# Performance work log

Measured on AMD Instinct MI355X. Metric: run time of the kernel, lower is better.

## Reference

```python
import jax, jax.numpy as jnp
import numpy as np

NEG = 0.01  # leaky_relu negative slope used throughout AttentiveFP


def _seg_softmax(logits, seg, num):
    # softmax over entries grouped by segment id (PyG softmax w/ 1e-16 eps)
    m = jax.ops.segment_max(logits, seg, num_segments=num)
    m = jnp.where(jnp.isfinite(m), m, 0.0)
    e = jnp.exp(logits - m[seg])
    s = jax.ops.segment_sum(e, seg, num_segments=num)
    return e / (s[seg] + 1e-16)


def _gru(x, h, wi, wh, bi, bh):
    # torch.nn.GRUCell math
    gi = x @ wi.T + bi
    gh = h @ wh.T + bh
    ir, iz, inn = jnp.split(gi, 3, axis=-1)
    hr, hz, hn = jnp.split(gh, 3, axis=-1)
    r = jax.nn.sigmoid(ir + hr)
    z = jax.nn.sigmoid(iz + hz)
    n = jnp.tanh(inn + r * hn)
    return (1.0 - z) * n + z * h


def _forward(x, edge_attr, mol_feats, lin1_w, lin1_b, gate_lin1_w, gate_lin2_w, gate_att_l, gate_att_r, gate_bias, grus_wi, grus_wh, grus_bi, grus_bh, atom_w, atom_att_src, atom_att_dst, atom_bias, mol_w, mol_att_src, mol_att_dst, mol_bias, lin2_w, lin2_b, fcm0_w, fcm0_b, fcm1_w, fcm1_b, fcm2_w, fcm2_b, fc0_w, fc0_b, fc1_w, fc1_b, fc2_w, fc2_b, fc3_w, fc3_b, fc4_w, fc4_b, edge_index, batch):
    N = x.shape[0]
    G = mol_feats.shape[0]
    src, dst = edge_index[0], edge_index[1]
    lrelu = lambda v: jax.nn.leaky_relu(v, NEG)
    # AttentiveFP (eval mode: dropout off)
    xh = lrelu(x @ lin1_w.T + lin1_b)  # [N,H]
    # --- GATEConv: edge-conditioned attention, add aggregation ---
    m = lrelu(jnp.concatenate([xh[src], edge_attr], axis=-1) @ gate_lin1_w.T)  # [E,H]
    a = lrelu(m @ gate_att_l + (xh @ gate_att_r)[dst])
    a = _seg_softmax(a, dst, N)
    h = jax.ops.segment_sum((m @ gate_lin2_w.T) * a[:, None], dst, num_segments=N) + gate_bias
    xh = jax.nn.relu(_gru(jax.nn.elu(h), xh, grus_wi[0], grus_wh[0], grus_bi[0], grus_bh[0]))
    # --- GATConv layers (num_layers-1 = 2, heads=1, no self loops) ---
    for l in range(2):
        xl = xh @ atom_w[l].T
        a = lrelu((xl @ atom_att_src[l])[src] + (xl @ atom_att_dst[l])[dst])
        a = _seg_softmax(a, dst, N)
        h = jax.ops.segment_sum(xl[src] * a[:, None], dst, num_segments=N) + atom_bias[l]
        xh = jax.nn.relu(_gru(jax.nn.elu(h), xh, grus_wi[1 + l], grus_wh[1 + l], grus_bi[1 + l], grus_bh[1 + l]))
    # --- attentive graph readout (num_timesteps = 3) ---
    out = jax.nn.relu(jax.ops.segment_sum(xh, batch, num_segments=G))  # [G,H]
    xm = xh @ mol_w.T            # atom-side lin (x fixed across timesteps)
    a_src = xm @ mol_att_src
    for _ in range(3):
        a = lrelu(a_src + ((out @ mol_w.T) @ mol_att_dst)[batch])
        a = _seg_softmax(a, batch, G)
        h = jax.ops.segment_sum(xm * a[:, None], batch, num_segments=G) + mol_bias
        out = jax.nn.relu(_gru(jax.nn.elu(h), out, grus_wi[3], grus_wh[3], grus_bi[3], grus_bh[3]))
    hg = out @ lin2_w.T + lin2_b  # [G,256]
    # --- mol-feature MLP branch (SiLU) ---
    hm = jax.nn.silu(mol_feats @ fcm0_w.T + fcm0_b)
    hm = jax.nn.silu(hm @ fcm1_w.T + fcm1_b)
    hm = jax.nn.silu(hm @ fcm2_w.T + fcm2_b)
    # --- fusion MLP ---
    hg = jnp.concatenate([hg, hm], axis=1)  # [G,512]
    hg = jax.nn.silu(hg @ fc0_w.T + fc0_b)
    hg = jax.nn.silu(hg @ fc1_w.T + fc1_b)
    hg = jax.nn.silu(hg @ fc2_w.T + fc2_b)
    hg = jax.nn.silu(hg @ fc3_w.T + fc3_b)
    return hg @ fc4_w.T + fc4_b  # [G,1]


def setup_inputs() -> dict:
    key = jax.random.key(0)
    ks = iter(jax.random.split(key, 64))
    def W(*shape):
        return jax.random.normal(next(ks), shape, jnp.float32) / np.float32(np.sqrt(shape[-1]))
    def B(*shape):
        return 0.02 * jax.random.normal(next(ks), shape, jnp.float32)
    N, E, G = 131072, 262144, 8192
    Fn, Fe, Fm, H = 64, 16, 200, 256
    return dict(
        x=jax.random.normal(next(ks), (N, Fn), jnp.float32),
        edge_attr=jax.random.normal(next(ks), (E, Fe), jnp.float32),
        mol_feats=jax.random.normal(next(ks), (G, Fm), jnp.float32),
        lin1_w=W(H, Fn), lin1_b=B(H),
        gate_lin1_w=W(H, H + Fe), gate_lin2_w=W(H, H),
        gate_att_l=W(H), gate_att_r=W(H), gate_bias=B(H),
        grus_wi=W(4, 3 * H, H), grus_wh=W(4, 3 * H, H), grus_bi=B(4, 3 * H), grus_bh=B(4, 3 * H),
        atom_w=W(2, H, H), atom_att_src=W(2, H), atom_att_dst=W(2, H), atom_bias=B(2, H),
        mol_w=W(H, H), mol_att_src=W(H), mol_att_dst=W(H), mol_bias=B(H),
        lin2_w=W(H, H), lin2_b=B(H),
        fcm0_w=W(H, Fm), fcm0_b=B(H), fcm1_w=W(H, H), fcm1_b=B(H), fcm2_w=W(H, H), fcm2_b=B(H),
        fc0_w=W(512, 512), fc0_b=B(512), fc1_w=W(512, 512), fc1_b=B(512),
        fc2_w=W(512, 512), fc2_b=B(512), fc3_w=W(128, 512), fc3_b=B(128),
        fc4_w=W(1, 128), fc4_b=B(1),
        edge_index=jax.random.randint(next(ks), (2, E), 0, N),
        batch=jnp.sort(jax.random.randint(next(ks), (N,), 0, G)),
    )


def reference(x, edge_attr, mol_feats, lin1_w, lin1_b, gate_lin1_w, gate_lin2_w, gate_att_l, gate_att_r, gate_bias, grus_wi, grus_wh, grus_bi, grus_bh, atom_w, atom_att_src, atom_att_dst, atom_bias, mol_w, mol_att_src, mol_att_dst, mol_bias, lin2_w, lin2_b, fcm0_w, fcm0_b, fcm1_w, fcm1_b, fcm2_w, fcm2_b, fc0_w, fc0_b, fc1_w, fc1_b, fc2_w, fc2_b, fc3_w, fc3_b, fc4_w, fc4_b, edge_index, batch):
    return _forward(x, edge_attr, mol_feats, lin1_w, lin1_b, gate_lin1_w, gate_lin2_w, gate_att_l, gate_att_r, gate_bias, grus_wi, grus_wh, grus_bi, grus_bh, atom_w, atom_att_src, atom_att_dst, atom_bias, mol_w, mol_att_src, mol_att_dst, mol_bias, lin2_w, lin2_b, fcm0_w, fcm0_b, fcm1_w, fcm1_b, fcm2_w, fcm2_b, fc0_w, fc0_b, fc1_w, fc1_b, fc2_w, fc2_b, fc3_w, fc3_b, fc4_w, fc4_b, edge_index, batch)
```

## Files before the change

kernel.cpp:

```cpp
#include <hip/hip_runtime.h>
#include <hip/hip_bf16.h>
#include <math.h>


typedef unsigned short u16;
typedef u16 u16x8 __attribute__((ext_vector_type(8)));
typedef short s16x8 __attribute__((ext_vector_type(8)));
typedef float f32x4 __attribute__((ext_vector_type(4)));

__device__ __forceinline__ float u2f(u16 u) { return __uint_as_float(((unsigned)u) << 16); }
__device__ __forceinline__ u16 f2u(float f) {
    return __builtin_bit_cast(u16, __float2bfloat16(f));
}

#define NEGS 0.01f

__device__ __forceinline__ unsigned fkey(float f) {
    unsigned u = __float_as_uint(f);
    return (u & 0x80000000u) ? ~u : (u | 0x80000000u);
}
__device__ __forceinline__ float funkey(unsigned k) {
    return (k & 0x80000000u) ? __uint_as_float(k ^ 0x80000000u) : __uint_as_float(~k);
}
#define KEY_NEG_INF 0x007FFFFFu

static inline int cdiv(int a, int b) { return (a + b - 1) / b; }

__global__ void fill_f32(float* p, float v, size_t n) {
    size_t i = (size_t)blockIdx.x * 256 + threadIdx.x;
    if (i < n) p[i] = v;
}
__global__ void fill_u32(unsigned* p, unsigned v, int n) {
    int i = blockIdx.x * 256 + threadIdx.x;
    if (i < n) p[i] = v;
}
__global__ void copy_f2b(const float* s, u16* d, size_t n) {
    size_t i = (size_t)blockIdx.x * 256 + threadIdx.x;
    if (i < n) d[i] = f2u(s[i]);
}
__global__ void copy_u32(const unsigned* s, unsigned* d, int n) {
    int i = blockIdx.x * 256 + threadIdx.x;
    if (i < n) d[i] = s[i];
}
__global__ void matvecT_k(const float* W, const float* a, float* v, int K, int Jout) {
    int j = blockIdx.x * 256 + threadIdx.x;
    if (j >= Jout) return;
    float s = 0.f;
    for (int k = 0; k < K; k++) s += W[(size_t)k * Jout + j] * a[k];
    v[j] = s;
}
__global__ void edge_add_lrelu(float* elog, const float* r, const int* dsti, int E) {
    int i = blockIdx.x * 256 + threadIdx.x;
    if (i < E) {
        float v = elog[i] + r[dsti[i]];
        elog[i] = v > 0.f ? v : NEGS * v;
    }
}
__global__ void pair_logit(float* elog, const float* s, const float* d,
                           const int* srci, const int* dsti, int E) {
    int i = blockIdx.x * 256 + threadIdx.x;
    if (i < E) {
        float v = s[srci[i]] + d[dsti[i]];
        elog[i] = v > 0.f ? v : NEGS * v;
    }
}
__global__ void node_logit(float* nlog, const float* asrc, const float* wg,
                           const int* batch, int N) {
    int i = blockIdx.x * 256 + threadIdx.x;
    if (i < N) {
        float v = asrc[i] + wg[batch[i]];
        nlog[i] = v > 0.f ? v : NEGS * v;
    }
}
__global__ void seg_max_k(const float* logit, const int* idx, unsigned* key, int n) {
    int i = blockIdx.x * 256 + threadIdx.x;
    if (i < n) atomicMax(&key[idx[i]], fkey(logit[i]));
}
__global__ void seg_exp_k(const float* logit, const int* idx, const unsigned* key,
                          float* ex, float* sum, int n) {
// ... 236 lines not shown
    if (ALD == 0) return sp_b(ab + k);
    if (ALD == 1) {
        if (k >= Ksrc) return sp_zero();
        return sp_f(af + k);
    }
    if (ALD == 2 || ALD == 5) {
        if (k < 256) return sp_b(ab + k);
        if (k < 272) return sp_f(x2 + (k - 256));
        return sp_zero();
    }
    if (ALD == 3) {
        if (k < 256) return sp_eluf(af + k);
        return sp_b(ab + (k - 256));
    }
    if (k < 256) return sp_eluf(af + k);
    return sp_f(x2 + (k - 256));
}
template <int ALD>
__device__ __forceinline__ bool lo_zero(int ki) {
    if (ALD == 0) return true;
    if (ALD == 2 || ALD == 5) return ki < 8;
    if (ALD == 3) return ki >= 8;
    return false;
}
template <int ACT>
__device__ __forceinline__ float actf(float v) {
    if (ACT == 1) return v > 0.f ? v : NEGS * v;
    if (ACT == 3) return v / (1.f + expf(-v));
    return v;
}

template <int ALD, int ACT, int EPI>
__global__ __launch_bounds__(256, 4) void mgemm(
    int M, int Kp, int Ksrc,
    const float* Af, int lda, const u16* Ab,
    const int* gidx, const int* sidx, const float* X2f, const u16* Wp,
    const float* b1,
    float* Cf, u16* Cb, int ldc,
    const float* attv, float* dotout) {
    __shared__ u16x8 lsAh[512];
    __shared__ u16x8 lsAl[512];
    __shared__ u16x8 lsWh[512];
    __shared__ u16x8 lsWl[512];
    const int t = threadIdx.x;
    const int m0 = blockIdx.x * 128;
    const int nb = blockIdx.y;
    const int kiters = Kp >> 5;
    const int r0 = ((t >> 6) << 4) | (t & 15);
    const int kq = ((t >> 4) & 3) << 3;
    const int mA[2] = {m0 + r0, m0 + r0 + 64};
    const u16* abr[2];
    const float* afr[2];
    const float* x2r[2];
    bool val[2];
#pragma unroll
    for (int h = 0; h < 2; h++) {
        int m = mA[h];
        val[h] = (m < M);
        int ms = val[h] ? m : 0;
        abr[h] = nullptr; afr[h] = nullptr; x2r[h] = nullptr;
        if (ALD == 0) {
            abr[h] = Ab + (size_t)ms * lda;
        } else if (ALD == 1) {
            afr[h] = Af + (size_t)ms * lda;
        } else if (ALD == 2) {
            abr[h] = Ab + (size_t)gidx[ms] * 256;
            x2r[h] = X2f + (size_t)ms * 16;
        } else if (ALD == 5) {
            int e = gidx[ms];
            abr[h] = Ab + (size_t)sidx[e] * 256;
            x2r[h] = X2f + (size_t)e * 16;
        } else if (ALD == 3) {
            afr[h] = Af + (size_t)ms * 256;
            abr[h] = Ab + (size_t)ms * 256;
        } else {
            afr[h] = Af + (size_t)ms * 256;
            x2r[h] = X2f + (size_t)ms * 256;
        }
    }
    const int wave = t >> 6, lane = t & 63;
    const int wm = (wave >> 1) << 6, wn = (wave & 1) << 6;
    f32x4 acc[4][4];
#pragma unroll
    for (int i = 0; i < 4; i++)
#pragma unroll
        for (int j = 0; j < 4; j++) {
            acc[i][j][0] = 0.f; acc[i][j][1] = 0.f; acc[i][j][2] = 0.f; acc[i][j][3] = 0.f;
        }
    const u16x8* wh0 = (const u16x8*)Wp + ((size_t)nb * kiters << 9);
    const u16x8* wl0 = wh0 + ((size_t)gridDim.y * kiters << 9);
    for (int ki = 0; ki < kiters; ki++) {
        int kb = (ki << 5) + kq;
        p8 a0 = ldA<ALD>(val[0], kb, Ksrc, abr[0], afr[0], x2r[0]);
        p8 a1 = ldA<ALD>(val[1], kb, Ksrc, abr[1], afr[1], x2r[1]);
        lsAh[t] = a0.hi; lsAl[t] = a0.lo;
        lsAh[t + 256] = a1.hi; lsAl[t + 256] = a1.lo;
        const u16x8* wsh = wh0 + ((size_t)ki << 9);
        const u16x8* wsl = wl0 + ((size_t)ki << 9);
        lsWh[t] = wsh[t]; lsWh[t + 256] = wsh[t + 256];
        lsWl[t] = wsl[t]; lsWl[t + 256] = wsl[t + 256];
        __syncthreads();
        s16x8 ah[4], al[4], wh[4], wl[4];
#pragma unroll
        for (int f = 0; f < 4; f++) {
            int ai = ((wm >> 4) + f) * 64 + lane;
            int wi = ((wn >> 4) + f) * 64 + lane;
            ah[f] = __builtin_bit_cast(s16x8, lsAh[ai]);
            al[f] = __builtin_bit_cast(s16x8, lsAl[ai]);
            wh[f] = __builtin_bit_cast(s16x8, lsWh[wi]);
            wl[f] = __builtin_bit_cast(s16x8, lsWl[wi]);
        }
        bool skip_lh = lo_zero<ALD>(ki);
#pragma unroll
        for (int fi = 0; fi < 4; fi++)
#pragma unroll
            for (int fj = 0; fj < 4; fj++) {
                acc[fi][fj] = __builtin_amdgcn_mfma_f32_16x16x32_bf16(
                    ah[fi], wh[fj], acc[fi][fj], 0, 0, 0);
                if (!skip_lh)
                    acc[fi][fj] = __builtin_amdgcn_mfma_f32_16x16x32_bf16(
                        al[fi], wh[fj], acc[fi][fj], 0, 0, 0);
                acc[fi][fj] = __builtin_amdgcn_mfma_f32_16x16x32_bf16(
                    ah[fi], wl[fj], acc[fi][fj], 0, 0, 0);
            }
        __syncthreads();
    }
    const int col = lane & 15, quad = lane >> 4;
    const int n_base = nb * 128 + wn;
    if (EPI == 2) {
        float dp[4][4] = {};
#pragma unroll
        for (int fi = 0; fi < 4; fi++)
#pragma unroll
            for (int fj = 0; fj < 4; fj++) {
                int nn = n_base + fj * 16 + col;
                float av = attv[nn];
#pragma unroll
                for (int r = 0; r < 4; r++) dp[fi][r] += actf<ACT>(acc[fi][fj][r]) * av;
            }
#pragma unroll
        for (int fi = 0; fi < 4; fi++)
#pragma unroll
            for (int r = 0; r < 4; r++) {
                float p = dp[fi][r];
                p += __shfl_down(p, 8);
                p += __shfl_down(p, 4);
                p += __shfl_down(p, 2);
                p += __shfl_down(p, 1);
                int mm = m0 + wm + fi * 16 + quad * 4 + r;
                if (col == 0 && mm < M) atomicAdd(dotout + mm, p);
            }
    } else {
#pragma unroll
        for (int fj = 0; fj < 4; fj++) {
            int nn = n_base + fj * 16 + col;
            float bb = b1 ? b1[nn] : 0.f;
#pragma unroll
            for (int fi = 0; fi < 4; fi++)
#pragma unroll
                for (int r = 0; r < 4; r++) {
                    int mm = m0 + wm + fi * 16 + quad * 4 + r;
                    if (mm >= M) continue;
                    float v = actf<ACT>(acc[fi][fj][r] + bb);
                    if (EPI == 1) Cb[(size_t)mm * ldc + nn] = f2u(v);
                    else Cf[(size_t)mm * ldc + nn] = v;
                }
        }
    }
}

template <int ALD, bool HB, bool OB>
__global__ __launch_bounds__(256, 4) void mgemm_gru(
    int M,
    const float* Af, const u16* Ab, const float* X2f,
    const u16* Wp, const float* bp,
    const u16* hb, const float* hf, float* of, u16* ob) {
    __shared__ u16x8 lsAh[512];
    __shared__ u16x8 lsAl[512];
    __shared__ u16x8 lsWh[512];
    __shared__ u16x8 lsWl[512];
    const int t = threadIdx.x;
    const int m0 = blockIdx.x * 128;
    const int nb = blockIdx.y;
    const int r0 = ((t >> 6) << 4) | (t & 15);
    const int kq = ((t >> 4) & 3) << 3;
    const int mA[2] = {m0 + r0, m0 + r0 + 64};
    const u16* abr[2];
    const float* afr[2];
    const float* x2r[2];
    bool val[2];
#pragma unroll
    for (int h = 0; h < 2; h++) {
        int m = mA[h];
        val[h] = (m < M);
        int ms = val[h] ? m : 0;
        abr[h] = nullptr; x2r[h] = nullptr;
        afr[h] = Af + (size_t)ms * 256;
        if (ALD == 3) abr[h] = Ab + (size_t)ms * 256;
        else x2r[h] = X2f + (size_t)ms * 256;
    }
    const int wave = t >> 6, lane = t & 63;
    const int wm = (wave >> 1) << 6, wn = (wave & 1) << 6;
    f32x4 acc[4][4];
#pragma unroll
    for (int i = 0; i < 4; i++)
#pragma unroll
        for (int j = 0; j < 4; j++) {
            acc[i][j][0] = 0.f; acc[i][j][1] = 0.f; acc[i][j][2] = 0.f; acc[i][j][3] = 0.f;
        }
    const u16x8* wh0 = (const u16x8*)Wp + ((size_t)nb * 16 << 9);
    const u16x8* wl0 = (const u16x8*)Wp + (size_t)(8 * 16 * 512) + ((size_t)nb * 16 << 9);
    for (int ki = 0; ki < 16; ki++) {
        int kb = (ki << 5) + kq;
        p8 a0 = ldA<ALD>(val[0], kb, 512, abr[0], afr[0], x2r[0]);
        p8 a1 = ldA<ALD>(val[1], kb, 512, abr[1], afr[1], x2r[1]);
        lsAh[t] = a0.hi; lsAl[t] = a0.lo;
        lsAh[t + 256] = a1.hi; lsAl[t + 256] = a1.lo;
        const u16x8* wsh = wh0 + ((size_t)ki << 9);
        const u16x8* wsl = wl0 + ((size_t)ki << 9);
        lsWh[t] = wsh[t]; lsWh[t + 256] = wsh[t + 256];
        lsWl[t] = wsl[t]; lsWl[t + 256] = wsl[t + 256];
        __syncthreads();
        s16x8 ah[4], al[4], wh[4], wl[4];
#pragma unroll
        for (int f = 0; f < 4; f++) {
            int ai = ((wm >> 4) + f) * 64 + lane;
            int wi = ((wn >> 4) + f) * 64 + lane;
            ah[f] = __builtin_bit_cast(s16x8, lsAh[ai]);
            al[f] = __builtin_bit_cast(s16x8, lsAl[ai]);
            wh[f] = __builtin_bit_cast(s16x8, lsWh[wi]);
            wl[f] = __builtin_bit_cast(s16x8, lsWl[wi]);
        }
        bool skip_lh = lo_zero<ALD>(ki);
        bool hn_zero = (ki < 8);
#pragma unroll
        for (int fi = 0; fi < 4; fi++)
#pragma unroll
            for (int fj = 0; fj < 4; fj++) {
                if (fj == 3 && hn_zero) continue;
                acc[fi][fj] = __builtin_amdgcn_mfma_f32_16x16x32_bf16(
                    ah[fi], wh[fj], acc[fi][fj], 0, 0, 0);
                if (!skip_lh)
                    acc[fi][fj] = __builtin_amdgcn_mfma_f32_16x16x32_bf16(
                        al[fi], wh[fj], acc[fi][fj], 0, 0, 0);
                acc[fi][fj] = __builtin_amdgcn_mfma_f32_16x16x32_bf16(
                    ah[fi], wl[fj], acc[fi][fj], 0, 0, 0);
            }
        __syncthreads();
    }
    const int col = lane & 15, quad = lane >> 4;
    const int nbase = nb * 128 + wn;
    float br = bp[nbase + col];
    float bz = bp[nbase + 16 + col];
    float bn = bp[nbase + 32 + col];
    float bhn = bp[nbase + 48 + col];
    int ch = (nb * 2 + (wn >> 6)) * 16 + col;
#pragma unroll
    for (int fi = 0; fi < 4; fi++)
#pragma unroll
        for (int r = 0; r < 4; r++) {
            int m = m0 + wm + fi * 16 + quad * 4 + r;
            if (m >= M) continue;
            float rs = acc[fi][0][r] + br;
            float zs = acc[fi][1][r] + bz;
            float nsv = acc[fi][2][r] + bn;
            float hnv = acc[fi][3][r] + bhn;
            float rr = 1.f / (1.f + expf(-rs));
            float zz = 1.f / (1.f + expf(-zs));
            float nn = tanhf(nsv - hnv + rr * hnv);
            float ho = HB ? u2f(hb[(size_t)m * 256 + ch]) : hf[(size_t)m * 256 + ch];
            float o = fmaxf((1.f - zz) * nn + zz * ho, 0.f);
            if (OB) ob[(size_t)m * 256 + ch] = f2u(o);
            else of[(size_t)m * 256 + ch] = o;
        }
}

extern "C" void kernel_launch(void* const* d_in, const int* in_sizes, int n_in,
                              void* d_out, int out_size, void* d_ws, size_t ws_size,
                              hipStream_t stream) {
    const float* x = (const float*)d_in[0];
    const float* edge_attr = (const float*)d_in[1];
    const float* mol_feats = (const float*)d_in[2];
    const float* lin1_w = (const float*)d_in[3];
    const float* lin1_b = (const float*)d_in[4];
    const float* gate_lin1_w = (const float*)d_in[5];
    const float* gate_lin2_w = (const float*)d_in[6];
    const float* gate_att_l = (const float*)d_in[7];
    const float* gate_att_r = (const float*)d_in[8];
    const float* gate_bias = (const float*)d_in[9];
    const float* grus_wi = (const float*)d_in[10];
    const float* grus_wh = (const float*)d_in[11];
    const float* grus_bi = (const float*)d_in[12];
    const float* grus_bh = (const float*)d_in[13];
    const float* atom_w = (const float*)d_in[14];
    const float* atom_att_src = (const float*)d_in[15];
    const float* atom_att_dst = (const float*)d_in[16];
    const float* atom_bias = (const float*)d_in[17];
    const float* mol_w = (const float*)d_in[18];
    const float* mol_att_src = (const float*)d_in[19];
    const float* mol_att_dst = (const float*)d_in[20];
    const float* mol_bias = (const float*)d_in[21];
    const float* lin2_w = (const float*)d_in[22];
    const float* lin2_b = (const float*)d_in[23];
    const float* fcm0_w = (const float*)d_in[24];
    const float* fcm0_b = (const float*)d_in[25];
    const float* fcm1_w = (const float*)d_in[26];
    const float* fcm1_b = (const float*)d_in[27];
// ... 112 lines not shown
        pack_gru_b<<<4, 256, 0, stream>>>(grus_bi + (size_t)l * 768,
                                          grus_bh + (size_t)l * 768, bp_gru[l]);
    }
    for (int l = 0; l < 2; l++)
        pack(atom_w + (size_t)l * 256 * 256, nullptr, 256, 256, 256, 256, pk_atom[l]);
    pack(mol_w, nullptr, 256, 256, 256, 256, pk_mol);
    pack(lin2_w, nullptr, 256, 256, 256, 256, pk_lin2);
    pack(fcm0_w, nullptr, 200, 200, 256, 224, pk_fcm0);
    pack(fcm1_w, nullptr, 256, 256, 256, 256, pk_fcm1);
    pack(fcm2_w, nullptr, 256, 256, 256, 256, pk_fcm2);
    pack(fc0_w, nullptr, 512, 512, 512, 512, pk_fc0);
    pack(fc1_w, nullptr, 512, 512, 512, 512, pk_fc1);
    pack(fc2_w, nullptr, 512, 512, 512, 512, pk_fc2);
    pack(fc3_w, nullptr, 512, 512, 128, 512, pk_fc3);

    fill_u32<<<cdiv(N, 256), 256, 0, stream>>>((unsigned*)ecnt, 0u, N);
    fill_u32<<<cdiv(N, 256), 256, 0, stream>>>((unsigned*)efill, 0u, N);
    fill_u32<<<1, 256, 0, stream>>>((unsigned*)cursor, 0u, 1);
    count_dst<<<cdiv(E, 256), 256, 0, stream>>>(dstE, ecnt, E);
    alloc_rows<<<cdiv(N, 256), 256, 0, stream>>>(ecnt, erowst, cursor, N);
    fill_csr<<<cdiv(E, 256), 256, 0, stream>>>(dstE, erowst, efill, eorder, E);
    fill_u32<<<cdiv(G, 256), 256, 0, stream>>>((unsigned*)gs, (unsigned)N, G);
    fill_u32<<<cdiv(G, 256), 256, 0, stream>>>((unsigned*)ge, 0u, G);
    graph_bounds<<<cdiv(N, 256), 256, 0, stream>>>(batch, gs, ge, N);

    u16* xh_cur = xhA;
    u16* xh_nxt = xhB;

    auto node_gru = [&](int l, const u16* Wpre, const float* bpre) {
        for (int c0 = 0; c0 < N; c0 += Mc) {
            int Ms = N - c0 < Mc ? N - c0 : Mc;
            int gx = cdiv(Ms, 128);
            if (hagg_f32)
                mgemm<1, 0, 0><<<dim3(gx, 2), 256, 0, stream>>>(Ms, 256, 256,
                    hagg32 + (size_t)c0 * 256, 256, nullptr, nullptr, nullptr,
                    nullptr, Wpre, bpre, cbuf, nullptr, 256, nullptr, nullptr);
            else
                mgemm<0, 0, 0><<<dim3(gx, 2), 256, 0, stream>>>(Ms, 256, 256,
                    nullptr, 256, hagg16 + (size_t)c0 * 256, nullptr, nullptr,
                    nullptr, Wpre, bpre, cbuf, nullptr, 256, nullptr, nullptr);
            if (use_pp)
                mgemm_gru<3, true, true><<<dim3(gx, 8), 256, 0, stream>>>(Ms,
                    cbuf, xh_cur + (size_t)c0 * 256, nullptr, pk_gruF[l], bp_gru[l],
                    xh_cur + (size_t)c0 * 256, nullptr, nullptr,
                    xh_nxt + (size_t)c0 * 256);
            else if (hagg_f32)
                mgemm_gru<3, true, false><<<dim3(gx, 8), 256, 0, stream>>>(Ms,
                    cbuf, xh_cur + (size_t)c0 * 256, nullptr, pk_gruF[l], bp_gru[l],
                    xh_cur + (size_t)c0 * 256, nullptr,
                    hagg32 + (size_t)c0 * 256, nullptr);
            else
                mgemm_gru<3, true, true><<<dim3(gx, 8), 256, 0, stream>>>(Ms,
                    cbuf, xh_cur + (size_t)c0 * 256, nullptr, pk_gruF[l], bp_gru[l],
                    xh_cur + (size_t)c0 * 256, nullptr, nullptr,
                    hagg16 + (size_t)c0 * 256);
        }
        if (use_pp) {
            u16* t2 = xh_cur; xh_cur = xh_nxt; xh_nxt = t2;
        } else if (hagg_f32) {
            copy_f2b<<<(int)(((size_t)N * 256 + 255) / 256), 256, 0, stream>>>(
                hagg32, xh_cur, (size_t)N * 256);
        } else {
            copy_u32<<<cdiv(N * 128, 256), 256, 0, stream>>>(
                (const unsigned*)hagg16, (unsigned*)xh_cur, N * 128);
        }
    };

    mgemm<1, 1, 1><<<dim3(cdiv(N, 128), 2), 256, 0, stream>>>(N, 64, 64,
        x, 64, nullptr, nullptr, nullptr, nullptr, pk_lin1, lin1_b,
        nullptr, xh_cur, 256, nullptr, nullptr);

    fill_f32<<<cdiv(E, 256), 256, 0, stream>>>(elog, 0.f, (size_t)E);
    mgemm<2, 1, 2><<<dim3(cdiv(E, 128), 2), 256, 0, stream>>>(E, 288, 272,
        nullptr, 0, xh_cur, srcE, nullptr, edge_attr, pk_g1, nullptr,
        nullptr, nullptr, 0, gate_att_l, elog);
    rowdot2_b<<<cdiv(N, 4), 256, 0, stream>>>(xh_cur, gate_att_r, nullptr, ns1, nullptr, N);
    edge_add_lrelu<<<cdiv(E, 256), 256, 0, stream>>>(elog, ns1, dstE, E);
    fill_u32<<<cdiv(N, 256), 256, 0, stream>>>(nkey, KEY_NEG_INF, N);
    fill_f32<<<cdiv(N, 256), 256, 0, stream>>>(nsum, 0.f, (size_t)N);
    seg_max_k<<<cdiv(E, 256), 256, 0, stream>>>(elog, dstE, nkey, E);
    seg_exp_k<<<cdiv(E, 256), 256, 0, stream>>>(elog, dstE, nkey, elog, nsum, E);
    seg_div_k<<<cdiv(E, 256), 256, 0, stream>>>(elog, dstE, nsum, aedge, E);
    if (hagg_f32)
        fill_f32<<<(int)(((size_t)N * 256 + 255) / 256), 256, 0, stream>>>(
            hagg32, 0.f, (size_t)N * 256);
    else
        fill_u32<<<cdiv(N * 128, 256), 256, 0, stream>>>((unsigned*)hagg16, 0u, N * 128);
    for (int c0 = 0; c0 < E; c0 += Ec) {
        int Ms = E - c0 < Ec ? E - c0 : Ec;
        mgemm<5, 1, 1><<<dim3(cdiv(Ms, 128), 2), 256, 0, stream>>>(Ms, 288, 272,
            nullptr, 0, xh_cur, eorder + c0, srcE, edge_attr, pk_g1, nullptr,
            nullptr, m_chunk, 256, nullptr, nullptr);
        if (hagg_f32)
            gate_csr_chunk<true><<<N, 256, 0, stream>>>(erowst, ecnt, eorder, aedge,
                m_chunk, hagg32, nullptr, N, c0, c0 + Ms);
        else
            gate_csr_chunk<false><<<N, 256, 0, stream>>>(erowst, ecnt, eorder, aedge,
                m_chunk, nullptr, hagg16, N, c0, c0 + Ms);
    }
    node_gru(0, pk_g2, gate_bias);

    for (int l = 0; l < 2; l++) {
        const float* aw = atom_w + (size_t)l * 256 * 256;
        matvecT_k<<<1, 256, 0, stream>>>(aw, atom_att_src + (size_t)l * 256, vbuf, 256, 256);
        matvecT_k<<<1, 256, 0, stream>>>(aw, atom_att_dst + (size_t)l * 256, vbuf + 256, 256, 256);
        rowdot2_b<<<cdiv(N, 4), 256, 0, stream>>>(xh_cur, vbuf, vbuf + 256, ns1, ns2, N);
        pair_logit<<<cdiv(E, 256), 256, 0, stream>>>(elog, ns1, ns2, srcE, dstE, E);
        fill_u32<<<cdiv(N, 256), 256, 0, stream>>>(nkey, KEY_NEG_INF, N);
        fill_f32<<<cdiv(N, 256), 256, 0, stream>>>(nsum, 0.f, (size_t)N);
        seg_max_k<<<cdiv(E, 256), 256, 0, stream>>>(elog, dstE, nkey, E);
        seg_exp_k<<<cdiv(E, 256), 256, 0, stream>>>(elog, dstE, nkey, elog, nsum, E);
        seg_div_k<<<cdiv(E, 256), 256, 0, stream>>>(elog, dstE, nsum, aedge, E);
        if (hagg_f32)
            csr_reduce_gat<true><<<N, 256, 0, stream>>>(erowst, ecnt, eorder, aedge,
                srcE, xh_cur, hagg32, nullptr, N);
        else
            csr_reduce_gat<false><<<N, 256, 0, stream>>>(erowst, ecnt, eorder, aedge,
                srcE, xh_cur, nullptr, hagg16, N);
        node_gru(1 + l, pk_atom[l], atom_bias + (size_t)l * 256);
    }

    seg_red<true><<<G, 256, 0, stream>>>(gs, ge, xh_cur, nullptr, outg, G);
    matvecT_k<<<1, 256, 0, stream>>>(mol_w, mol_att_dst, vbuf, 256, 256);
    matvecT_k<<<1, 256, 0, stream>>>(mol_w, mol_att_src, vbuf + 256, 256, 256);
    rowdot2_b<<<cdiv(N, 4), 256, 0, stream>>>(xh_cur, vbuf + 256, nullptr, ns1, nullptr, N);
    float* ogc = outg;
    float* ogn = hgrb;
    int McG = Mc < G ? Mc : G;
    for (int t = 0; t < 3; t++) {
        rowdot_f<<<cdiv(G, 4), 256, 0, stream>>>(ogc, vbuf, wgb, G);
        node_logit<<<cdiv(N, 256), 256, 0, stream>>>(elog, ns1, wgb, batch, N);
        fill_u32<<<cdiv(G, 256), 256, 0, stream>>>(gkey, KEY_NEG_INF, G);
        fill_f32<<<cdiv(G, 256), 256, 0, stream>>>(gsum, 0.f, (size_t)G);
        seg_max_k<<<cdiv(N, 256), 256, 0, stream>>>(elog, batch, gkey, N);
        seg_exp_k<<<cdiv(N, 256), 256, 0, stream>>>(elog, batch, gkey, elog, gsum, N);
        seg_div_k<<<cdiv(N, 256), 256, 0, stream>>>(elog, batch, gsum, aedge, N);
        seg_red<false><<<G, 256, 0, stream>>>(gs, ge, xh_cur, aedge, ogn, G);
        for (int c0 = 0; c0 < G; c0 += McG) {
            int Ms = G - c0 < McG ? G - c0 : McG;
            int gx = cdiv(Ms, 128);
            mgemm<1, 0, 0><<<dim3(gx, 2), 256, 0, stream>>>(Ms, 256, 256,
                ogn + (size_t)c0 * 256, 256, nullptr, nullptr, nullptr, nullptr,
                pk_mol, mol_bias, cbuf, nullptr, 256, nullptr, nullptr);
            mgemm_gru<4, false, false><<<dim3(gx, 8), 256, 0, stream>>>(Ms,
                cbuf, nullptr, ogc + (size_t)c0 * 256, pk_gruF[3], bp_gru[3],
                nullptr, ogc + (size_t)c0 * 256, ogn + (size_t)c0 * 256, nullptr);
        }
        float* tt = ogc; ogc = ogn; ogn = tt;
    }

    int gG = cdiv(G, 128);
    mgemm<1, 3, 0><<<dim3(gG, 2), 256, 0, stream>>>(G, 224, 200, mol_feats, 200,
        nullptr, nullptr, nullptr, nullptr, pk_fcm0, fcm0_b,
        hm1, nullptr, 256, nullptr, nullptr);
    mgemm<1, 3, 0><<<dim3(gG, 2), 256, 0, stream>>>(G, 256, 256, hm1, 256,
        nullptr, nullptr, nullptr, nullptr, pk_fcm1, fcm1_b,
        hm2, nullptr, 256, nullptr, nullptr);
    mgemm<1, 3, 0><<<dim3(gG, 2), 256, 0, stream>>>(G, 256, 256, hm2, 256,
        nullptr, nullptr, nullptr, nullptr, pk_fcm2, fcm2_b,
        fbufA + 256, nullptr, 512, nullptr, nullptr);
    mgemm<1, 0, 0><<<dim3(gG, 2), 256, 0, stream>>>(G, 256, 256, ogc, 256,
        nullptr, nullptr, nullptr, nullptr, pk_lin2, lin2_b,
        fbufA, nullptr, 512, nullptr, nullptr);
    mgemm<1, 3, 0><<<dim3(gG, 4), 256, 0, stream>>>(G, 512, 512, fbufA, 512,
        nullptr, nullptr, nullptr, nullptr, pk_fc0, fc0_b,
        fbufB, nullptr, 512, nullptr, nullptr);
    mgemm<1, 3, 0><<<dim3(gG, 4), 256, 0, stream>>>(G, 512, 512, fbufB, 512,
        nullptr, nullptr, nullptr, nullptr, pk_fc1, fc1_b,
        fbufC, nullptr, 512, nullptr, nullptr);
    mgemm<1, 3, 0><<<dim3(gG, 4), 256, 0, stream>>>(G, 512, 512, fbufC, 512,
        nullptr, nullptr, nullptr, nullptr, pk_fc2, fc2_b,
        fbufB, nullptr, 512, nullptr, nullptr);
    mgemm<1, 3, 0><<<dim3(gG, 1), 256, 0, stream>>>(G, 512, 512, fbufB, 512,
        nullptr, nullptr, nullptr, nullptr, pk_fc3, fc3_b,
        f128, nullptr, 128, nullptr, nullptr);
    fc4_k<<<cdiv(G, 4), 256, 0, stream>>>(f128, fc4_w, fc4_b, out_final, G);
}
```

Baseline: 6.524 ms.

## Loop over N-blocks inside GEMM blocks and merge small init/matvec launches

The GEMM and GRU-GEMM kernels gain an NBL parameter so one thread block walks several output column blocks in turn instead of each column block getting its own grid slice. For the large node and edge GEMMs the grid y-dimension drops to 1, so the A-row gather (including the edge gather of xh) is held in the same block across all column tiles, though A is still reloaded per column tile. The EPI==2 path now accumulates the attention dot across column tiles before a single atomicAdd, and it can optionally write the activations. Separately, fill pairs are fused into one init_softmax kernel and two matvec launches into one two-slice launch. The cost is fewer blocks and less parallelism per launch, plus more serial work per block.

```diff
diff --git a/kernel.cpp b/kernel.cpp
--- a/kernel.cpp
+++ b/kernel.cpp
@@ -34,6 +34,13 @@
     int i = blockIdx.x * 256 + threadIdx.x;
     if (i < n) p[i] = v;
 }
+__global__ void init_softmax(unsigned* key, float* sum, int n) {
+    int i = blockIdx.x * 256 + threadIdx.x;
+    if (i < n) {
+        key[i] = KEY_NEG_INF;
+        sum[i] = 0.f;
+    }
+}
 __global__ void copy_f2b(const float* s, u16* d, size_t n) {
     size_t i = (size_t)blockIdx.x * 256 + threadIdx.x;
     if (i < n) d[i] = f2u(s[i]);
@@ -42,9 +49,12 @@
     int i = blockIdx.x * 256 + threadIdx.x;
     if (i < n) d[i] = s[i];
 }
-__global__ void matvecT_k(const float* W, const float* a, float* v, int K, int Jout) {
+__global__ void matvecT2_k(const float* W, const float* a0, const float* a1,
+                           float* v0, float* v1, int K, int Jout) {
     int j = blockIdx.x * 256 + threadIdx.x;
     if (j >= Jout) return;
+    const float* a = blockIdx.y ? a1 : a0;
+    float* v = blockIdx.y ? v1 : v0;
     float s = 0.f;
     for (int k = 0; k < K; k++) s += W[(size_t)k * Jout + j] * a[k];
     v[j] = s;
@@ -347,7 +357,7 @@
 
 template <int ALD, int ACT, int EPI>
 __global__ __launch_bounds__(256, 4) void mgemm(
-    int M, int Kp, int Ksrc,
+    int M, int Kp, int Ksrc, int NBT, int NBL,
     const float* Af, int lda, const u16* Ab,
     const int* gidx, const int* sidx, const float* X2f, const u16* Wp,
     const float* b1,
@@ -359,7 +369,7 @@
     __shared__ u16x8 lsWl[512];
     const int t = threadIdx.x;
     const int m0 = blockIdx.x * 128;
-    const int nb = blockIdx.y;
+    const int nb0 = blockIdx.y * NBL;
     const int kiters = Kp >> 5;
     const int r0 = ((t >> 6) << 4) | (t & 15);
     const int kq = ((t >> 4) & 3) << 3;
@@ -395,64 +405,94 @@
     }
     const int wave = t >> 6, lane = t & 63;
     const int wm = (wave >> 1) << 6, wn = (wave & 1) << 6;
-    f32x4 acc[4][4];
-#pragma unroll
-    for (int i = 0; i < 4; i++)
-#pragma unroll
-        for (int j = 0; j < 4; j++) {
-            acc[i][j][0] = 0.f; acc[i][j][1] = 0.f; acc[i][j][2] = 0.f; acc[i][j][3] = 0.f;
+    const int col = lane & 15, quad = lane >> 4;
+    float dp[4][4] = {};
+    for (int nbi = 0; nbi < NBL; nbi++) {
+        int nb = nb0 + nbi;
+        f32x4 acc[4][4];
+#pragma unroll
+        for (int i = 0; i < 4; i++)
+#pragma unroll
+            for (int j = 0; j < 4; j++) {
+                acc[i][j][0] = 0.f; acc[i][j][1] = 0.f;
+                acc[i][j][2] = 0.f; acc[i][j][3] = 0.f;
+            }
+        const u16x8* wh0 = (const u16x8*)Wp + ((size_t)nb * kiters << 9);
+        const u16x8* wl0 = (const u16x8*)Wp + (((size_t)NBT * kiters) << 9) +
+                           ((size_t)nb * kiters << 9);
+        for (int ki = 0; ki < kiters; ki++) {
+            int kb = (ki << 5) + kq;
+            p8 a0 = ldA<ALD>(val[0], kb, Ksrc, abr[0], afr[0], x2r[0]);
+            p8 a1 = ldA<ALD>(val[1], kb, Ksrc, abr[1], afr[1], x2r[1]);
+            lsAh[t] = a0.hi; lsAl[t] = a0.lo;
+            lsAh[t + 256] = a1.hi; lsAl[t + 256] = a1.lo;
+            const u16x8* wsh = wh0 + ((size_t)ki << 9);
+            const u16x8* wsl = wl0 + ((size_t)ki << 9);
+            lsWh[t] = wsh[t]; lsWh[t + 256] = wsh[t + 256];
+            lsWl[t] = wsl[t]; lsWl[t + 256] = wsl[t + 256];
+            __syncthreads();
+            s16x8 ah[4], al[4], wh[4], wl[4];
+#pragma unroll
+            for (int f = 0; f < 4; f++) {
+                int ai = ((wm >> 4) + f) * 64 + lane;
+                int wi = ((wn >> 4) + f) * 64 + lane;
+                ah[f] = __builtin_bit_cast(s16x8, lsAh[ai]);
+                al[f] = __builtin_bit_cast(s16x8, lsAl[ai]);
+                wh[f] = __builtin_bit_cast(s16x8, lsWh[wi]);
+                wl[f] = __builtin_bit_cast(s16x8, lsWl[wi]);
+            }
+            bool skip_lh = lo_zero<ALD>(ki);
+#pragma unroll
+            for (int fi = 0; fi < 4; fi++)
+#pragma unroll
+                for (int fj = 0; fj < 4; fj++) {
+                    acc[fi][fj] = __builtin_amdgcn_mfma_f32_16x16x32_bf16(
+                        ah[fi], wh[fj], acc[fi][fj], 0, 0, 0);
+                    if (!skip_lh)
+                        acc[fi][fj] = __builtin_amdgcn_mfma_f32_16x16x32_bf16(
+                            al[fi], wh[fj], acc[fi][fj], 0, 0, 0);
+                    acc[fi][fj] = __builtin_amdgcn_mfma_f32_16x16x32_bf16(
+                        ah[fi], wl[fj], acc[fi][fj], 0, 0, 0);
+                }
+            __syncthreads();
         }
-    const u16x8* wh0 = (const u16x8*)Wp + ((size_t)nb * kiters << 9);
-    const u16x8* wl0 = wh0 + ((size_t)gridDim.y * kiters << 9);
-    for (int ki = 0; ki < kiters; ki++) {
-        int kb = (ki << 5) + kq;
-        p8 a0 = ldA<ALD>(val[0], kb, Ksrc, abr[0], afr[0], x2r[0]);
-        p8 a1 = ldA<ALD>(val[1], kb, Ksrc, abr[1], afr[1], x2r[1]);
-        lsAh[t] = a0.hi; lsAl[t] = a0.lo;
-        lsAh[t + 256] = a1.hi; lsAl[t + 256] = a1.lo;
-        const u16x8* wsh = wh0 + ((size_t)ki << 9);
-        const u16x8* wsl = wl0 + ((size_t)ki << 9);
-        lsWh[t] = wsh[t]; lsWh[t + 256] = wsh[t + 256];
-        lsWl[t] = wsl[t]; lsWl[t + 256] = wsl[t + 256];
-        __syncthreads();
-        s16x8 ah[4], al[4], wh[4], wl[4];
-#pragma unroll
-        for (int f = 0; f < 4; f++) {
-            int ai = ((wm >> 4) + f) * 64 + lane;
-            int wi = ((wn >> 4) + f) * 64 + lane;
-            ah[f] = __builtin_bit_cast(s16x8, lsAh[ai]);
-            al[f] = __builtin_bit_cast(s16x8, lsAl[ai]);
-            wh[f] = __builtin_bit_cast(s16x8, lsWh[wi]);
-            wl[f] = __builtin_bit_cast(s16x8, lsWl[wi]);
-        }
-        bool skip_lh = lo_zero<ALD>(ki);
-#pragma unroll
-        for (int fi = 0; fi < 4; fi++)
-#pragma unroll
-            for (int fj = 0; fj < 4; fj++) {
-                acc[fi][fj] = __builtin_amdgcn_mfma_f32_16x16x32_bf16(
-                    ah[fi], wh[fj], acc[fi][fj], 0, 0, 0);
-                if (!skip_lh)
-                    acc[fi][fj] = __builtin_amdgcn_mfma_f32_16x16x32_bf16(
-                        al[fi], wh[fj], acc[fi][fj], 0, 0, 0);
-                acc[fi][fj] = __builtin_amdgcn_mfma_f32_16x16x32_bf16(
-                    ah[fi], wl[fj], acc[fi][fj], 0, 0, 0);
-            }
-        __syncthreads();
-    }
-    const int col = lane & 15, quad = lane >> 4;
-    const int n_base = nb * 128 + wn;
-    if (EPI == 2) {
-        float dp[4][4] = {};
-#pragma unroll
-        for (int fi = 0; fi < 4; fi++)
+        const int n_base = nb * 128 + wn;
+        if (EPI == 2) {
+#pragma unroll
+            for (int fi = 0; fi < 4; fi++)
+#pragma unroll
+                for (int fj = 0; fj < 4; fj++) {
+                    int nn = n_base + fj * 16 + col;
+                    float av = attv[nn];
+#pragma unroll
+                    for (int r = 0; r < 4; r++) {
+                        float v = actf<ACT>(acc[fi][fj][r]);
+                        dp[fi][r] += v * av;
+                        if (Cb) {
+                            int mm = m0 + wm + fi * 16 + quad * 4 + r;
+                            if (mm < M) Cb[(size_t)mm * ldc + nn] = f2u(v);
+                        }
+                    }
+                }
+        } else {
 #pragma unroll
             for (int fj = 0; fj < 4; fj++) {
                 int nn = n_base + fj * 16 + col;
-                float av = attv[nn];
-#pragma unroll
-                for (int r = 0; r < 4; r++) dp[fi][r] += actf<ACT>(acc[fi][fj][r]) * av;
+                float bb = b1 ? b1[nn] : 0.f;
+#pragma unroll
+                for (int fi = 0; fi < 4; fi++)
+#pragma unroll
+                    for (int r = 0; r < 4; r++) {
+                        int mm = m0 + wm + fi * 16 + quad * 4 + r;
+                        if (mm >= M) continue;
+                        float v = actf<ACT>(acc[fi][fj][r] + bb);
+                        if (EPI == 1) Cb[(size_t)mm * ldc + nn] = f2u(v);
+                        else Cf[(size_t)mm * ldc + nn] = v;
+                    }
             }
+        }
+    }
+    if (EPI == 2) {
 #pragma unroll
         for (int fi = 0; fi < 4; fi++)
 #pragma unroll
@@ -465,28 +505,12 @@
                 int mm = m0 + wm + fi * 16 + quad * 4 + r;
                 if (col == 0 && mm < M) atomicAdd(dotout + mm, p);
             }
-    } else {
-#pragma unroll
-        for (int fj = 0; fj < 4; fj++) {
-            int nn = n_base + fj * 16 + col;
-            float bb = b1 ? b1[nn] : 0.f;
-#pragma unroll
-            for (int fi = 0; fi < 4; fi++)
-#pragma unroll
-                for (int r = 0; r < 4; r++) {
-                    int mm = m0 + wm + fi * 16 + quad * 4 + r;
-                    if (mm >= M) continue;
-                    float v = actf<ACT>(acc[fi][fj][r] + bb);
-                    if (EPI == 1) Cb[(size_t)mm * ldc + nn] = f2u(v);
-                    else Cf[(size_t)mm * ldc + nn] = v;
-                }
-        }
     }
 }
 
 template <int ALD, bool HB, bool OB>
 __global__ __launch_bounds__(256, 4) void mgemm_gru(
-    int M,
+    int M, int NBL,
     const float* Af, const u16* Ab, const float* X2f,
     const u16* Wp, const float* bp,
     const u16* hb, const float* hf, float* of, u16* ob) {
@@ -496,7 +520,7 @@
     __shared__ u16x8 lsWl[512];
     const int t = threadIdx.x;
     const int m0 = blockIdx.x * 128;
-    const int nb = blockIdx.y;
+    const int nb0 = blockIdx.y * NBL;
     const int r0 = ((t >> 6) << 4) | (t & 15);
     const int kq = ((t >> 4) & 3) << 3;
     const int mA[2] = {m0 + r0, m0 + r0 + 64};
@@ -516,78 +540,84 @@
     }
     const int wave = t >> 6, lane = t & 63;
     const int wm = (wave >> 1) << 6, wn = (wave & 1) << 6;
-    f32x4 acc[4][4];
-#pragma unroll
-    for (int i = 0; i < 4; i++)
-#pragma unroll
-        for (int j = 0; j < 4; j++) {
-            acc[i][j][0] = 0.f; acc[i][j][1] = 0.f; acc[i][j][2] = 0.f; acc[i][j][3] = 0.f;
+    const int col = lane & 15, quad = lane >> 4;
+    for (int nbi = 0; nbi < NBL; nbi++) {
+        int nb = nb0 + nbi;
+        f32x4 acc[4][4];
+#pragma unroll
+        for (int i = 0; i < 4; i++)
+#pragma unroll
+            for (int j = 0; j < 4; j++) {
+                acc[i][j][0] = 0.f; acc[i][j][1] = 0.f;
+                acc[i][j][2] = 0.f; acc[i][j][3] = 0.f;
+            }
+        const u16x8* wh0 = (const u16x8*)Wp + ((size_t)nb * 16 << 9);
+        const u16x8* wl0 = (const u16x8*)Wp + (size_t)(8 * 16 * 512) +
+                           ((size_t)nb * 16 << 9);
+        for (int ki = 0; ki < 16; ki++) {
+            int kb = (ki << 5) + kq;
+            p8 a0 = ldA<ALD>(val[0], kb, 512, abr[0], afr[0], x2r[0]);
+            p8 a1 = ldA<ALD>(val[1], kb, 512, abr[1], afr[1], x2r[1]);
+            lsAh[t] = a0.hi; lsAl[t] = a0.lo;
+            lsAh[t + 256] = a1.hi; lsAl[t + 256] = a1.lo;
+            const u16x8* wsh = wh0 + ((size_t)ki << 9);
+            const u16x8* wsl = wl0 + ((size_t)ki << 9);
+            lsWh[t] = wsh[t]; lsWh[t + 256] = wsh[t + 256];
+            lsWl[t] = wsl[t]; lsWl[t + 256] = wsl[t + 256];
+            __syncthreads();
+            s16x8 ah[4], al[4], wh[4], wl[4];
+#pragma unroll
+            for (int f = 0; f < 4; f++) {
+                int ai = ((wm >> 4) + f) * 64 + lane;
+                int wi = ((wn >> 4) + f) * 64 + lane;
+                ah[f] = __builtin_bit_cast(s16x8, lsAh[ai]);
+                al[f] = __builtin_bit_cast(s16x8, lsAl[ai]);
+                wh[f] = __builtin_bit_cast(s16x8, lsWh[wi]);
+                wl[f] = __builtin_bit_cast(s16x8, lsWl[wi]);
+            }
+            bool skip_lh = lo_zero<ALD>(ki);
+            bool hn_zero = (ki < 8);
+#pragma unroll
+            for (int fi = 0; fi < 4; fi++)
+#pragma unroll
+                for (int fj = 0; fj < 4; fj++) {
+                    if (fj == 3 && hn_zero) continue;
+                    acc[fi][fj] = __builtin_amdgcn_mfma_f32_16x16x32_bf16(
+                        ah[fi], wh[fj], acc[fi][fj], 0, 0, 0);
+                    if (!skip_lh)
+                        acc[fi][fj] = __builtin_amdgcn_mfma_f32_16x16x32_bf16(
+                            al[fi], wh[fj], acc[fi][fj], 0, 0, 0);
+                    acc[fi][fj] = __builtin_amdgcn_mfma_f32_16x16x32_bf16(
+                        ah[fi], wl[fj], acc[fi][fj], 0, 0, 0);
+                }
+            __syncthreads();
         }
-    const u16x8* wh0 = (const u16x8*)Wp + ((size_t)nb * 16 << 9);
-    const u16x8* wl0 = (const u16x8*)Wp + (size_t)(8 * 16 * 512) + ((size_t)nb * 16 << 9);
-    for (int ki = 0; ki < 16; ki++) {
-        int kb = (ki << 5) + kq;
-        p8 a0 = ldA<ALD>(val[0], kb, 512, abr[0], afr[0], x2r[0]);
-        p8 a1 = ldA<ALD>(val[1], kb, 512, abr[1], afr[1], x2r[1]);
-        lsAh[t] = a0.hi; lsAl[t] = a0.lo;
-        lsAh[t + 256] = a1.hi; lsAl[t + 256] = a1.lo;
-        const u16x8* wsh = wh0 + ((size_t)ki << 9);
-        const u16x8* wsl = wl0 + ((size_t)ki << 9);
-        lsWh[t] = wsh[t]; lsWh[t + 256] = wsh[t + 256];
-        lsWl[t] = wsl[t]; lsWl[t + 256] = wsl[t + 256];
-        __syncthreads();
-        s16x8 ah[4], al[4], wh[4], wl[4];
-#pragma unroll
-        for (int f = 0; f < 4; f++) {
-            int ai = ((wm >> 4) + f) * 64 + lane;
-            int wi = ((wn >> 4) + f) * 64 + lane;
-            ah[f] = __builtin_bit_cast(s16x8, lsAh[ai]);
-            al[f] = __builtin_bit_cast(s16x8, lsAl[ai]);
-            wh[f] = __builtin_bit_cast(s16x8, lsWh[wi]);
-            wl[f] = __builtin_bit_cast(s16x8, lsWl[wi]);
-        }
-        bool skip_lh = lo_zero<ALD>(ki);
-        bool hn_zero = (ki < 8);
+        const int nbase = nb * 128 + wn;
+        float br = bp[nbase + col];
+        float bz = bp[nbase + 16 + col];
+        float bn = bp[nbase + 32 + col];
+        float bhn = bp[nbase + 48 + col];
+        int ch = (nb * 2 + (wn >> 6)) * 16 + col;
 #pragma unroll
         for (int fi = 0; fi < 4; fi++)
 #pragma unroll
-            for (int fj = 0; fj < 4; fj++) {
-                if (fj == 3 && hn_zero) continue;
-                acc[fi][fj] = __builtin_amdgcn_mfma_f32_16x16x32_bf16(
-                    ah[fi], wh[fj], acc[fi][fj], 0, 0, 0);
-                if (!skip_lh)
-                    acc[fi][fj] = __builtin_amdgcn_mfma_f32_16x16x32_bf16(
-                        al[fi], wh[fj], acc[fi][fj], 0, 0, 0);
-                acc[fi][fj] = __builtin_amdgcn_mfma_f32_16x16x32_bf16(
-                    ah[fi], wl[fj], acc[fi][fj], 0, 0, 0);
+            for (int r = 0; r < 4; r++) {
+                int m = m0 + wm + fi * 16 + quad * 4 + r;
+                if (m >= M) continue;
+                float rs = acc[fi][0][r] + br;
+                float zs = acc[fi][1][r] + bz;
+                float nsv = acc[fi][2][r] + bn;
+                float hnv = acc[fi][3][r] + bhn;
+                float rr = 1.f / (1.f + expf(-rs));
+                float zz = 1.f / (1.f + expf(-zs));
+                float nn = tanhf(nsv - hnv + rr * hnv);
+                float ho = HB ? u2f(hb[(size_t)m * 256 + ch])
+                              : hf[(size_t)m * 256 + ch];
+                float o = fmaxf((1.f - zz) * nn + zz * ho, 0.f);
+                if (OB) ob[(size_t)m * 256 + ch] = f2u(o);
+                else of[(size_t)m * 256 + ch] = o;
             }
-        __syncthreads();
-    }
-    const int col = lane & 15, quad = lane >> 4;
-    const int nbase = nb * 128 + wn;
-    float br = bp[nbase + col];
-    float bz = bp[nbase + 16 + col];
-    float bn = bp[nbase + 32 + col];
-    float bhn = bp[nbase + 48 + col];
-    int ch = (nb * 2 + (wn >> 6)) * 16 + col;
-#pragma unroll
-    for (int fi = 0; fi < 4; fi++)
-#pragma unroll
-        for (int r = 0; r < 4; r++) {
-            int m = m0 + wm + fi * 16 + quad * 4 + r;
-            if (m >= M) continue;
-            float rs = acc[fi][0][r] + br;
-            float zs = acc[fi][1][r] + bz;
-            float nsv = acc[fi][2][r] + bn;
-            float hnv = acc[fi][3][r] + bhn;
-            float rr = 1.f / (1.f + expf(-rs));
-            float zz = 1.f / (1.f + expf(-zs));
-            float nn = tanhf(nsv - hnv + rr * hnv);
-            float ho = HB ? u2f(hb[(size_t)m * 256 + ch]) : hf[(size_t)m * 256 + ch];
-            float o = fmaxf((1.f - zz) * nn + zz * ho, 0.f);
-            if (OB) ob[(size_t)m * 256 + ch] = f2u(o);
-            else of[(size_t)m * 256 + ch] = o;
-        }
+    }
 }
 
 extern "C" void kernel_launch(void* const* d_in, const int* in_sizes, int n_in,
@@ -766,25 +796,25 @@
             int Ms = N - c0 < Mc ? N - c0 : Mc;
             int gx = cdiv(Ms, 128);
             if (hagg_f32)
-                mgemm<1, 0, 0><<<dim3(gx, 2), 256, 0, stream>>>(Ms, 256, 256,
+                mgemm<1, 0, 0><<<dim3(gx, 1), 256, 0, stream>>>(Ms, 256, 256, 2, 2,
                     hagg32 + (size_t)c0 * 256, 256, nullptr, nullptr, nullptr,
                     nullptr, Wpre, bpre, cbuf, nullptr, 256, nullptr, nullptr);
             else
-                mgemm<0, 0, 0><<<dim3(gx, 2), 256, 0, stream>>>(Ms, 256, 256,
+                mgemm<0, 0, 0><<<dim3(gx, 1), 256, 0, stream>>>(Ms, 256, 256, 2, 2,
                     nullptr, 256, hagg16 + (size_t)c0 * 256, nullptr, nullptr,
                     nullptr, Wpre, bpre, cbuf, nullptr, 256, nullptr, nullptr);
             if (use_pp)
-                mgemm_gru<3, true, true><<<dim3(gx, 8), 256, 0, stream>>>(Ms,
+                mgemm_gru<3, true, true><<<dim3(gx, 1), 256, 0, stream>>>(Ms, 8,
                     cbuf, xh_cur + (size_t)c0 * 256, nullptr, pk_gruF[l], bp_gru[l],
                     xh_cur + (size_t)c0 * 256, nullptr, nullptr,
                     xh_nxt + (size_t)c0 * 256);
             else if (hagg_f32)
-                mgemm_gru<3, true, false><<<dim3(gx, 8), 256, 0, stream>>>(Ms,
+                mgemm_gru<3, true, false><<<dim3(gx, 1), 256, 0, stream>>>(Ms, 8,
                     cbuf, xh_cur + (size_t)c0 * 256, nullptr, pk_gruF[l], bp_gru[l],
                     xh_cur + (size_t)c0 * 256, nullptr,
                     hagg32 + (size_t)c0 * 256, nullptr);
             else
-                mgemm_gru<3, true, true><<<dim3(gx, 8), 256, 0, stream>>>(Ms,
+                mgemm_gru<3, true, true><<<dim3(gx, 1), 256, 0, stream>>>(Ms, 8,
                     cbuf, xh_cur + (size_t)c0 * 256, nullptr, pk_gruF[l], bp_gru[l],
                     xh_cur + (size_t)c0 * 256, nullptr, nullptr,
                     hagg16 + (size_t)c0 * 256);
@@ -800,18 +830,17 @@
         }
     };
 
-    mgemm<1, 1, 1><<<dim3(cdiv(N, 128), 2), 256, 0, stream>>>(N, 64, 64,
+    mgemm<1, 1, 1><<<dim3(cdiv(N, 128), 1), 256, 0, stream>>>(N, 64, 64, 2, 2,
         x, 64, nullptr, nullptr, nullptr, nullptr, pk_lin1, lin1_b,
         nullptr, xh_cur, 256, nullptr, nullptr);
 
     fill_f32<<<cdiv(E, 256), 256, 0, stream>>>(elog, 0.f, (size_t)E);
-    mgemm<2, 1, 2><<<dim3(cdiv(E, 128), 2), 256, 0, stream>>>(E, 288, 272,
+    mgemm<2, 1, 2><<<dim3(cdiv(E, 128), 1), 256, 0, stream>>>(E, 288, 272, 2, 2,
         nullptr, 0, xh_cur, srcE, nullptr, edge_attr, pk_g1, nullptr,
         nullptr, nullptr, 0, gate_att_l, elog);
     rowdot2_b<<<cdiv(N, 4), 256, 0, stream>>>(xh_cur, gate_att_r, nullptr, ns1, nullptr, N);
     edge_add_lrelu<<<cdiv(E, 256), 256, 0, stream>>>(elog, ns1, dstE, E);
-    fill_u32<<<cdiv(N, 256), 256, 0, stream>>>(nkey, KEY_NEG_INF, N);
-    fill_f32<<<cdiv(N, 256), 256, 0, stream>>>(nsum, 0.f, (size_t)N);
+    init_softmax<<<cdiv(N, 256), 256, 0, stream>>>(nkey, nsum, N);
     seg_max_k<<<cdiv(E, 256), 256, 0, stream>>>(elog, dstE, nkey, E);
     seg_exp_k<<<cdiv(E, 256), 256, 0, stream>>>(elog, dstE, nkey, elog, nsum, E);
     seg_div_k<<<cdiv(E, 256), 256, 0, stream>>>(elog, dstE, nsum, aedge, E);
@@ -822,7 +851,7 @@
         fill_u32<<<cdiv(N * 128, 256), 256, 0, stream>>>((unsigned*)hagg16, 0u, N * 128);
     for (int c0 = 0; c0 < E; c0 += Ec) {
         int Ms = E - c0 < Ec ? E - c0 : Ec;
-        mgemm<5, 1, 1><<<dim3(cdiv(Ms, 128), 2), 256, 0, stream>>>(Ms, 288, 272,
+        mgemm<5, 1, 1><<<dim3(cdiv(Ms, 128), 1), 256, 0, stream>>>(Ms, 288, 272, 2, 2,
             nullptr, 0, xh_cur, eorder + c0, srcE, edge_attr, pk_g1, nullptr,
             nullptr, m_chunk, 256, nullptr, nullptr);
         if (hagg_f32)
@@ -836,12 +865,12 @@
 
     for (int l = 0; l < 2; l++) {
         const float* aw = atom_w + (size_t)l * 256 * 256;
-        matvecT_k<<<1, 256, 0, stream>>>(aw, atom_att_src + (size_t)l * 256, vbuf, 256, 256);
-        matvecT_k<<<1, 256, 0, stream>>>(aw, atom_att_dst + (size_t)l * 256, vbuf + 256, 256, 256);
+        matvecT2_k<<<dim3(1, 2), 256, 0, stream>>>(aw,
+            atom_att_src + (size_t)l * 256, atom_att_dst + (size_t)l * 256,
+            vbuf, vbuf + 256, 256, 256);
         rowdot2_b<<<cdiv(N, 4), 256, 0, stream>>>(xh_cur, vbuf, vbuf + 256, ns1, ns2, N);
         pair_logit<<<cdiv(E, 256), 256, 0, stream>>>(elog, ns1, ns2, srcE, dstE, E);
-        fill_u32<<<cdiv(N, 256), 256, 0, stream>>>(nkey, KEY_NEG_INF, N);
-        fill_f32<<<cdiv(N, 256), 256, 0, stream>>>(nsum, 0.f, (size_t)N);
+        init_softmax<<<cdiv(N, 256), 256, 0, stream>>>(nkey, nsum, N);
         seg_max_k<<<cdiv(E, 256), 256, 0, stream>>>(elog, dstE, nkey, E);
         seg_exp_k<<<cdiv(E, 256), 256, 0, stream>>>(elog, dstE, nkey, elog, nsum, E);
         seg_div_k<<<cdiv(E, 256), 256, 0, stream>>>(elog, dstE, nsum, aedge, E);
@@ -855,8 +884,8 @@
     }
 
     seg_red<true><<<G, 256, 0, stream>>>(gs, ge, xh_cur, nullptr, outg, G);
-    matvecT_k<<<1, 256, 0, stream>>>(mol_w, mol_att_dst, vbuf, 256, 256);
-    matvecT_k<<<1, 256, 0, stream>>>(mol_w, mol_att_src, vbuf + 256, 256, 256);
+    matvecT2_k<<<dim3(1, 2), 256, 0, stream>>>(mol_w, mol_att_dst, mol_att_src,
+                                               vbuf, vbuf + 256, 256, 256);
     rowdot2_b<<<cdiv(N, 4), 256, 0, stream>>>(xh_cur, vbuf + 256, nullptr, ns1, nullptr, N);
     float* ogc = outg;
     float* ogn = hgrb;
@@ -864,8 +893,7 @@
     for (int t = 0; t < 3; t++) {
         rowdot_f<<<cdiv(G, 4), 256, 0, stream>>>(ogc, vbuf, wgb, G);
         node_logit<<<cdiv(N, 256), 256, 0, stream>>>(elog, ns1, wgb, batch, N);
-        fill_u32<<<cdiv(G, 256), 256, 0, stream>>>(gkey, KEY_NEG_INF, G);
-        fill_f32<<<cdiv(G, 256), 256, 0, stream>>>(gsum, 0.f, (size_t)G);
+        init_softmax<<<cdiv(G, 256), 256, 0, stream>>>(gkey, gsum, G);
         seg_max_k<<<cdiv(N, 256), 256, 0, stream>>>(elog, batch, gkey, N);
         seg_exp_k<<<cdiv(N, 256), 256, 0, stream>>>(elog, batch, gkey, elog, gsum, N);
         seg_div_k<<<cdiv(N, 256), 256, 0, stream>>>(elog, batch, gsum, aedge, N);
@@ -873,10 +901,10 @@
         for (int c0 = 0; c0 < G; c0 += McG) {
             int Ms = G - c0 < McG ? G - c0 : McG;
             int gx = cdiv(Ms, 128);
-            mgemm<1, 0, 0><<<dim3(gx, 2), 256, 0, stream>>>(Ms, 256, 256,
+            mgemm<1, 0, 0><<<dim3(gx, 2), 256, 0, stream>>>(Ms, 256, 256, 2, 1,
                 ogn + (size_t)c0 * 256, 256, nullptr, nullptr, nullptr, nullptr,
                 pk_mol, mol_bias, cbuf, nullptr, 256, nullptr, nullptr);
-            mgemm_gru<4, false, false><<<dim3(gx, 8), 256, 0, stream>>>(Ms,
+            mgemm_gru<4, false, false><<<dim3(gx, 8), 256, 0, stream>>>(Ms, 1,
                 cbuf, nullptr, ogc + (size_t)c0 * 256, pk_gruF[3], bp_gru[3],
                 nullptr, ogc + (size_t)c0 * 256, ogn + (size_t)c0 * 256, nullptr);
         }
@@ -884,29 +912,29 @@
     }
 
     int gG = cdiv(G, 128);
-    mgemm<1, 3, 0><<<dim3(gG, 2), 256, 0, stream>>>(G, 224, 200, mol_feats, 200,
-        nullptr, nullptr, nullptr, nullptr, pk_fcm0, fcm0_b,
+    mgemm<1, 3, 0><<<dim3(gG, 2), 256, 0, stream>>>(G, 224, 200, 2, 1,
+        mol_feats, 200, nullptr, nullptr, nullptr, nullptr, pk_fcm0, fcm0_b,
         hm1, nullptr, 256, nullptr, nullptr);
-    mgemm<1, 3, 0><<<dim3(gG, 2), 256, 0, stream>>>(G, 256, 256, hm1, 256,
-        nullptr, nullptr, nullptr, nullptr, pk_fcm1, fcm1_b,
+    mgemm<1, 3, 0><<<dim3(gG, 2), 256, 0, stream>>>(G, 256, 256, 2, 1,
+        hm1, 256, nullptr, nullptr, nullptr, nullptr, pk_fcm1, fcm1_b,
         hm2, nullptr, 256, nullptr, nullptr);
-    mgemm<1, 3, 0><<<dim3(gG, 2), 256, 0, stream>>>(G, 256, 256, hm2, 256,
-        nullptr, nullptr, nullptr, nullptr, pk_fcm2, fcm2_b,
+    mgemm<1, 3, 0><<<dim3(gG, 2), 256, 0, stream>>>(G, 256, 256, 2, 1,
+        hm2, 256, nullptr, nullptr, nullptr, nullptr, pk_fcm2, fcm2_b,
         fbufA + 256, nullptr, 512, nullptr, nullptr);
-    mgemm<1, 0, 0><<<dim3(gG, 2), 256, 0, stream>>>(G, 256, 256, ogc, 256,
-        nullptr, nullptr, nullptr, nullptr, pk_lin2, lin2_b,
+    mgemm<1, 0, 0><<<dim3(gG, 2), 256, 0, stream>>>(G, 256, 256, 2, 1,
+        ogc, 256, nullptr, nullptr, nullptr, nullptr, pk_lin2, lin2_b,
         fbufA, nullptr, 512, nullptr, nullptr);
-    mgemm<1, 3, 0><<<dim3(gG, 4), 256, 0, stream>>>(G, 512, 512, fbufA, 512,
-        nullptr, nullptr, nullptr, nullptr, pk_fc0, fc0_b,
+    mgemm<1, 3, 0><<<dim3(gG, 4), 256, 0, stream>>>(G, 512, 512, 4, 1,
+        fbufA, 512, nullptr, nullptr, nullptr, nullptr, pk_fc0, fc0_b,
         fbufB, nullptr, 512, nullptr, nullptr);
-    mgemm<1, 3, 0><<<dim3(gG, 4), 256, 0, stream>>>(G, 512, 512, fbufB, 512,
-        nullptr, nullptr, nullptr, nullptr, pk_fc1, fc1_b,
+    mgemm<1, 3, 0><<<dim3(gG, 4), 256, 0, stream>>>(G, 512, 512, 4, 1,
+        fbufB, 512, nullptr, nullptr, nullptr, nullptr, pk_fc1, fc1_b,
         fbufC, nullptr, 512, nullptr, nullptr);
-    mgemm<1, 3, 0><<<dim3(gG, 4), 256, 0, stream>>>(G, 512, 512, fbufC, 512,
-        nullptr, nullptr, nullptr, nullptr, pk_fc2, fc2_b,
+    mgemm<1, 3, 0><<<dim3(gG, 4), 256, 0, stream>>>(G, 512, 512, 4, 1,
+        fbufC, 512, nullptr, nullptr, nullptr, nullptr, pk_fc2, fc2_b,
         fbufB, nullptr, 512, nullptr, nullptr);
-    mgemm<1, 3, 0><<<dim3(gG, 1), 256, 0, stream>>>(G, 512, 512, fbufB, 512,
-        nullptr, nullptr, nullptr, nullptr, pk_fc3, fc3_b,
+    mgemm<1, 3, 0><<<dim3(gG, 1), 256, 0, stream>>>(G, 512, 512, 1, 1,
+        fbufB, 512, nullptr, nullptr, nullptr, nullptr, pk_fc3, fc3_b,
         f128, nullptr, 128, nullptr, nullptr);
     fc4_k<<<cdiv(G, 4), 256, 0, stream>>>(f128, fc4_w, fc4_b, out_final, G);
 }
```

Measured after the change: 10.76 ms. +65.0%, slower.
